# Optimization experiments

Hardware: AMD Instinct MI355X
Metric: run time of the kernel (lower is better)

Reference implementation:

```python
import jax, jax.numpy as jnp
import numpy as np
from jax import lax

SR = 4      # sr_ratio
HEADS = 8   # num_heads


def _upsample_bilinear_ac(x, out_h, out_w):
    # torch nn.Upsample(scale_factor=SR, mode='bilinear', align_corners=True)
    B, C, h, w = x.shape
    ys = jnp.linspace(0.0, h - 1.0, out_h)
    xs = jnp.linspace(0.0, w - 1.0, out_w)
    y0 = jnp.floor(ys).astype(jnp.int32)
    y1 = jnp.minimum(y0 + 1, h - 1)
    wy = (ys - y0).astype(x.dtype)
    x0 = jnp.floor(xs).astype(jnp.int32)
    x1 = jnp.minimum(x0 + 1, w - 1)
    wx = (xs - x0).astype(x.dtype)
    r = x[:, :, y0, :] * (1.0 - wy)[None, None, :, None] + x[:, :, y1, :] * wy[None, None, :, None]
    return r[:, :, :, x0] * (1.0 - wx) + r[:, :, :, x1] * wx


def _forward(x, sr_w, sr_b, ln_g, ln_b, q_w, k1_w, v1_w, k2_w, v2_w, proj_w, proj_b):
    B, C, H, W = x.shape
    ID = C // 4                      # internal_dim
    hd = ID // HEADS                 # head_dim
    scale = float(hd) ** -0.5
    # spatial-reduction conv for Q path: [B, ID, H/4, W/4]
    qf = lax.conv_general_dilated(x, sr_w, (SR, SR), 'VALID',
                                  dimension_numbers=('NCHW', 'OIHW', 'NCHW'))
    qf = qf + sr_b[None, :, None, None]
    Hs, Ws = qf.shape[2], qf.shape[3]
    N = Hs * Ws
    qf = qf.reshape(B, ID, N).transpose(0, 2, 1)          # [B, N, ID]
    # LayerNorm
    mu = qf.mean(-1, keepdims=True)
    var = qf.var(-1, keepdims=True)
    qn = (qf - mu) / jnp.sqrt(var + 1e-5) * ln_g + ln_b
    q = qn @ q_w                                          # [B, N, ID]
    # max / avg pooled K,V inputs: [B, N, C]
    xm = lax.reduce_window(x, -jnp.inf, lax.max, (1, 1, SR, SR), (1, 1, SR, SR), 'VALID')
    xm = xm.reshape(B, C, N).transpose(0, 2, 1)
    xa = lax.reduce_window(x, 0.0, lax.add, (1, 1, SR, SR), (1, 1, SR, SR), 'VALID') / float(SR * SR)
    xa = xa.reshape(B, C, N).transpose(0, 2, 1)

    def heads(t):
        return t.reshape(B, N, HEADS, hd).transpose(0, 2, 1, 3)  # [B, H, N, hd]

    qh = heads(q)
    k1, v1 = heads(xm @ k1_w), heads(xm @ v1_w)
    k2, v2 = heads(xa @ k2_w), heads(xa @ v2_w)

    def attend(k, v):
        a = jax.nn.softmax(jnp.einsum('bhnd,bhmd->bhnm', qh, k) * scale, axis=-1)
        return jnp.einsum('bhnm,bhmd->bhnd', a, v)

    z = attend(k1, v1) + attend(k2, v2)                   # [B, H, N, hd]
    z = z.transpose(0, 2, 1, 3).reshape(B, N, ID)
    z = z @ proj_w + proj_b                               # [B, N, C]
    z = z.transpose(0, 2, 1).reshape(B, C, Hs, Ws)
    return _upsample_bilinear_ac(z, H, W)


def setup_inputs() -> dict:
    key = jax.random.key(0)
    ks = jax.random.split(key, 9)
    B, C, H, W = 16, 256, 112, 112
    ID = C // 4

    def n(k, shape, s=0.02):
        return jax.random.normal(k, shape, jnp.float32) * s

    return {
        'x': jax.random.normal(ks[0], (B, C, H, W), jnp.float32),
        'sr_w': n(ks[1], (ID, C, SR, SR)),
        'sr_b': jnp.zeros((ID,), jnp.float32),
        'ln_g': jnp.ones((ID,), jnp.float32),
        'ln_b': jnp.zeros((ID,), jnp.float32),
        'q_w': n(ks[2], (ID, ID)),
        'k1_w': n(ks[3], (C, ID)),
        'v1_w': n(ks[4], (C, ID)),
        'k2_w': n(ks[5], (C, ID)),
        'v2_w': n(ks[6], (C, ID)),
        'proj_w': n(ks[7], (ID, C)),
        'proj_b': jnp.zeros((C,), jnp.float32),
    }


def reference(x, sr_w, sr_b, ln_g, ln_b, q_w, k1_w, v1_w, k2_w, v2_w, proj_w, proj_b):
    return _forward(x, sr_w, sr_b, ln_g, ln_b, q_w, k1_w, v1_w, k2_w, v2_w, proj_w, proj_b)
```

## Files before the change

### kernel.cpp

```cpp
#include <hip/hip_runtime.h>
#include <math.h>

typedef __attribute__((ext_vector_type(8))) short short8;
typedef __attribute__((ext_vector_type(4))) short bh4;
typedef __attribute__((ext_vector_type(4))) float f32x4;
typedef __attribute__((ext_vector_type(2))) unsigned uint2v;
typedef __attribute__((ext_vector_type(4))) unsigned uint4v;

#define MFMA16(A,B,C) __builtin_amdgcn_mfma_f32_16x16x32_bf16(A,B,C,0,0,0)

#if __has_builtin(__builtin_amdgcn_mfma_f32_16x16x16bf16_1k)
#define MFMA16x16(A,B,C) __builtin_amdgcn_mfma_f32_16x16x16bf16_1k(A,B,C,0,0,0)
#else
__device__ __forceinline__ f32x4 mfma16x16_asm(bh4 a, bh4 b, f32x4 c){
    asm volatile("v_mfma_f32_16x16x16_bf16 %0, %1, %2, %0" : "+v"(c) : "v"(a), "v"(b));
    return c;
}
#define MFMA16x16(A,B,C) mfma16x16_asm(A,B,C)
#endif

__device__ __forceinline__ unsigned short f2b(float f){
    unsigned u = __builtin_bit_cast(unsigned, f);
    return (unsigned short)((u + 0x7fffu + ((u>>16)&1u)) >> 16);
}
__device__ __forceinline__ unsigned pk2(float a, float b){
    return (unsigned)f2b(a) | ((unsigned)f2b(b) << 16);
}
__device__ __forceinline__ unsigned pk2rn(float a, float b){
    unsigned ua = __builtin_bit_cast(unsigned, a) + 0x8000u;
    unsigned ub = __builtin_bit_cast(unsigned, b) + 0x8000u;
    return (ua >> 16) | (ub & 0xffff0000u);
}


__global__ __launch_bounds__(256) void ktw(const float* __restrict__ srw,
    const float* __restrict__ qw, const float* __restrict__ k1w,
    const float* __restrict__ v1w, const float* __restrict__ k2w,
    const float* __restrict__ v2w, char* __restrict__ srwb,
    char* __restrict__ Wtm, char* __restrict__ Wta, char* __restrict__ QWt)
{
    int blk = blockIdx.x, t = threadIdx.x;
    if (blk < 128){
        int base = blk*2048 + t*8;
        float4 a = *(const float4*)(srw + base);
        float4 b = *(const float4*)(srw + base + 4);
        uint4 u = { pk2(a.x,a.y), pk2(a.z,a.w), pk2(b.x,b.y), pk2(b.z,b.w) };
        *(uint4*)(srwb + (size_t)base*2) = u;
    } else if (blk < 136){
        __shared__ float T[256*33];
        int idx = blk - 128, fi = idx >> 1, half = idx & 1;
        const float* src = (fi==0) ? k1w : (fi==1) ? v1w : (fi==2) ? k2w : v2w;
        char* dst = ((fi < 2) ? Wtm : Wta) + (size_t)((fi & 1)*64 + half*32) * 512;
        for (int li = t; li < 8192; li += 256){
            int c = li >> 5, o = li & 31;
            T[c*33 + o] = src[c*64 + half*32 + o];
        }
        __syncthreads();
        for (int lo = t; lo < 1024; lo += 256){
            int o = lo >> 5, c8 = lo & 31;
            float v[8];
            #pragma unroll
            for (int k = 0; k < 8; ++k) v[k] = T[(c8*8 + k)*33 + o];
            uint4 u = { pk2(v[0],v[1]), pk2(v[2],v[3]), pk2(v[4],v[5]), pk2(v[6],v[7]) };
            *(uint4*)(dst + o*512 + c8*16) = u;
        }
    } else {
        __shared__ float T[64*65];
        for (int li = t; li < 4096; li += 256)
            T[(li >> 6)*65 + (li & 63)] = qw[li];
        __syncthreads();
        for (int lo = t; lo < 512; lo += 256){
            int o = lo >> 3, i8 = lo & 7;
            float v[8];
            #pragma unroll
            for (int k = 0; k < 8; ++k) v[k] = T[(i8*8 + k)*65 + o];
            uint4 u = { pk2(v[0],v[1]), pk2(v[2],v[3]), pk2(v[4],v[5]), pk2(v[6],v[7]) };
            *(uint4*)(QWt + o*128 + i8*16) = u;
        }
    }
}

__global__ __launch_bounds__(256, 4) void k1(const float* __restrict__ x,
    const char* __restrict__ srwb, char* __restrict__ R, float* __restrict__ pws)
{
    __shared__ float pm[28*66];
    __shared__ float pa[28*66];
    int blk = blockIdx.x;
    int b = blk / 112, r5 = blk % 112, hs = r5 >> 2, cg4 = r5 & 3;
    int t = threadIdx.x;
    int w = t >> 6, l = t & 63, lr = l & 15, lg = l >> 4;
    int cpar = lg >> 1, r0 = (lg & 1) * 2;
    f32x4 acc0 = {0.f,0.f,0.f,0.f}, acc1 = {0.f,0.f,0.f,0.f};
    const float* xc = x + (size_t)(b*256 + cg4*64)*12544 + (size_t)(hs*4 + r0)*112;
    const char* Brow = srwb + (size_t)(w*16 + lr)*8192 + cg4*2048 + lg*16;
    int p0 = lr, p1 = min(16 + lr, 27);

    f32x4 A0,A1,A2,A3; uint4v Ba;
    f32x4 C0,C1,C2,C3; uint4v Bc;
    f32x4 D0,D1,D2,D3; uint4v Bd;
    f32x4 E0,E1,E2,E3; uint4v Be;

#define ISSUE(Xa,Xb,Xc,Xd,Bv,KS) do{ \
    const float* _s = xc + (size_t)((KS)*2 + cpar)*12544; \
    const char*  _bp = Brow + (KS)*64; \
    asm volatile("global_load_dwordx4 %0, %1, off" : "=&v"(Xa) : "v"(_s + p0*4)); \
    asm volatile("global_load_dwordx4 %0, %1, off" : "=&v"(Xb) : "v"(_s + 112 + p0*4)); \
    asm volatile("global_load_dwordx4 %0, %1, off" : "=&v"(Xc) : "v"(_s + p1*4)); \
    asm volatile("global_load_dwordx4 %0, %1, off" : "=&v"(Xd) : "v"(_s + 112 + p1*4)); \
    asm volatile("global_load_dwordx4 %0, %1, off" : "=&v"(Bv) : "v"(_bp)); }while(0)

#define WAITN(N) do{ asm volatile("s_waitcnt vmcnt(" #N ")" ::: "memory"); \
                     __builtin_amdgcn_sched_barrier(0); }while(0)

#define COMP(Xa,Xb,Xc,Xd,Bv,KS) do{ \
    if (w == 0){ \
        float mx0 = fmaxf(fmaxf(fmaxf(Xa[0],Xa[1]),fmaxf(Xa[2],Xa[3])), \
                          fmaxf(fmaxf(Xb[0],Xb[1]),fmaxf(Xb[2],Xb[3]))); \
        float sm0 = (Xa[0]+Xa[1])+(Xa[2]+Xa[3])+(Xb[0]+Xb[1])+(Xb[2]+Xb[3]); \
        float mx1 = fmaxf(fmaxf(fmaxf(Xc[0],Xc[1]),fmaxf(Xc[2],Xc[3])), \
                          fmaxf(fmaxf(Xd[0],Xd[1]),fmaxf(Xd[2],Xd[3]))); \
        float sm1 = (Xc[0]+Xc[1])+(Xc[2]+Xc[3])+(Xd[0]+Xd[1])+(Xd[2]+Xd[3]); \
        mx0 = fmaxf(mx0, __shfl_xor(mx0, 16, 64)); \
        sm0 = sm0 + __shfl_xor(sm0, 16, 64); \
        mx1 = fmaxf(mx1, __shfl_xor(mx1, 16, 64)); \
        sm1 = sm1 + __shfl_xor(sm1, 16, 64); \
        if ((lg & 1) == 0){ \
            int c = (KS)*2 + cpar; \
            pm[p0*66 + c] = mx0; pa[p0*66 + c] = sm0 * (1.f/16.f); \
            if (lr < 12){ pm[p1*66 + c] = mx1; pa[p1*66 + c] = sm1 * (1.f/16.f); } \
        } \
    } \
    short8 af0 = __builtin_bit_cast(short8, \
        (uint4v){ pk2(Xa[0],Xa[1]), pk2(Xa[2],Xa[3]), pk2(Xb[0],Xb[1]), pk2(Xb[2],Xb[3]) }); \
    short8 af1 = __builtin_bit_cast(short8, \
        (uint4v){ pk2(Xc[0],Xc[1]), pk2(Xc[2],Xc[3]), pk2(Xd[0],Xd[1]), pk2(Xd[2],Xd[3]) }); \
    short8 bf = __builtin_bit_cast(short8, Bv); \
    acc0 = MFMA16(af0, bf, acc0); \
    acc1 = MFMA16(af1, bf, acc1); }while(0)

    ISSUE(A0,A1,A2,A3,Ba, 0);
    ISSUE(C0,C1,C2,C3,Bc, 1);
    ISSUE(D0,D1,D2,D3,Bd, 2);
    ISSUE(E0,E1,E2,E3,Be, 3);
    #pragma unroll 1
    for (int it = 0; it < 7; ++it){
        int s4 = it*4;
        WAITN(15); COMP(A0,A1,A2,A3,Ba, s4+0); ISSUE(A0,A1,A2,A3,Ba, s4+4);
        WAITN(15); COMP(C0,C1,C2,C3,Bc, s4+1); ISSUE(C0,C1,C2,C3,Bc, s4+5);
        WAITN(15); COMP(D0,D1,D2,D3,Bd, s4+2); ISSUE(D0,D1,D2,D3,Bd, s4+6);
        WAITN(15); COMP(E0,E1,E2,E3,Be, s4+3); ISSUE(E0,E1,E2,E3,Be, s4+7);
    }
    WAITN(15); COMP(A0,A1,A2,A3,Ba, 28);
    WAITN(10); COMP(C0,C1,C2,C3,Bc, 29);
    WAITN(5);  COMP(D0,D1,D2,D3,Bd, 30);
    WAITN(0);  COMP(E0,E1,E2,E3,Be, 31);

#undef ISSUE
#undef WAITN
#undef COMP

    size_t rowB = (size_t)b*784 + hs*28;
    float* pp = pws + (size_t)((b*28 + hs)*4 + cg4)*1792;
    #pragma unroll
    for (int rg = 0; rg < 4; ++rg){
        int m0 = lg*4 + rg, m1 = 16 + lg*4 + rg;
        pp[m0*64 + w*16 + lr] = acc0[rg];
        if (m1 < 28) pp[m1*64 + w*16 + lr] = acc1[rg];
    }
    __syncthreads();
    if (t < 224){
        int m = t >> 3, sub = t & 7;
        float vm[8], va8[8];
        #pragma unroll
        for (int k = 0; k < 8; ++k){
            vm[k]  = pm[m*66 + sub*8 + k];
            va8[k] = pa[m*66 + sub*8 + k];
        }
        uint4 um = { pk2(vm[0],vm[1]), pk2(vm[2],vm[3]), pk2(vm[4],vm[5]), pk2(vm[6],vm[7]) };
        uint4 ua = { pk2(va8[0],va8[1]), pk2(va8[2],va8[3]), pk2(va8[4],va8[5]), pk2(va8[6],va8[7]) };
        *(uint4*)(R + (rowB + m)*1024 + cg4*128 + sub*16)       = um;
        *(uint4*)(R + (rowB + m)*1024 + 512 + cg4*128 + sub*16) = ua;
    }
}

__global__ __launch_bounds__(512) void k2(const float* __restrict__ pws_,
    const float* __restrict__ srb, const float* __restrict__ lng,
    const float* __restrict__ lnb, const char* __restrict__ Wtm,
    const char* __restrict__ Wta, const char* __restrict__ QWt,
    char* __restrict__ R)
{
    __shared__ __align__(16) char PM[16384];
    __shared__ __align__(16) char PA[16384];
    __shared__ float Db[32*64];
    __shared__ __align__(16) char QN[4096];
    int blk = blockIdx.x, b = blk/28, hs = blk%28;
    int t = threadIdx.x, w = t>>6, l = t&63, lr = l&15, lg = l>>4;
    size_t rowB = (size_t)b*784 + hs*28;
    const char* Rb = R + rowB*1024;
    for (int li = t; li < 896; li += 512){
        int m = li >> 5, c16 = li & 31;
        uint4 vm = *(const uint4*)(Rb + (size_t)m*1024 + c16*16);
        uint4 va = *(const uint4*)(Rb + (size_t)m*1024 + 512 + c16*16);
        int dst = m*512 + ((c16*16) ^ ((m&7)<<4));
        *(uint4*)(PM + dst) = vm;
        *(uint4*)(PA + dst) = va;
    }
    const float* p0 = pws_ + (size_t)(b*28 + hs)*4*1792;
    for (int e = t; e < 1792; e += 512)
        Db[e] = ((p0[e] + p0[1792+e]) + (p0[3584+e] + p0[5376+e])) + srb[e & 63];
    __syncthreads();
    float g = lng[l], be = lnb[l];
    #pragma unroll
    for (int i = 0; i < 4; ++i){
        int m = w + i*8;
        float v = Db[m*64 + l];
        float s = v, ss = v*v;
        #pragma unroll
        for (int off = 1; off < 64; off <<= 1){
            s  += __shfl_xor(s,  off, 64);
            ss += __shfl_xor(ss, off, 64);
        }
        float mu = s * (1.f/64.f);
        float var = ss * (1.f/64.f) - mu*mu;
        float qn = (v - mu) * rsqrtf(var + 1e-5f) * g + be;
        *(unsigned short*)(QN + m*128 + ((l*2) ^ ((m&7)<<4))) = f2b(qn);
    }
    __syncthreads();
    int fam = w >> 2, ofp = w & 3;
    const char* PMA = fam ? PA : PM;
    const char* Wt  = fam ? Wta : Wtm;
    f32x4 a00={0.f,0.f,0.f,0.f}, a01=a00, a10=a00, a11=a00;
    int swzr = (lr & 7) << 4;
    #pragma unroll
    for (int ks = 0; ks < 8; ++ks){
        int kb = ks*64 + lg*16;
        short8 x0 = *(const short8*)(PMA + lr*512 + (kb ^ swzr));
        short8 x1 = *(const short8*)(PMA + (16+lr)*512 + (kb ^ swzr));
        short8 b0 = *(const short8*)(Wt + (size_t)(ofp*32 + lr)*512 + kb);
        short8 b1 = *(const short8*)(Wt + (size_t)(ofp*32 + 16 + lr)*512 + kb);
        a00 = MFMA16(x0, b0, a00); a01 = MFMA16(x0, b1, a01);
        a10 = MFMA16(x1, b0, a10); a11 = MFMA16(x1, b1, a11);
    }
    f32x4 q0={0.f,0.f,0.f,0.f}, q1=q0;
    if (w < 4){
        #pragma unroll
        for (int ks = 0; ks < 2; ++ks){
            int kb = ks*64 + lg*16;
            short8 xa_ = *(const short8*)(QN + lr*128 + (kb ^ swzr));
            short8 xb_ = *(const short8*)(QN + (16+lr)*128 + (kb ^ swzr));
            short8 bq  = *(const short8*)(QWt + (size_t)(w*16 + lr)*128 + kb);
            q0 = MFMA16(xa_, bq, q0);
            q1 = MFMA16(xb_, bq, q1);
        }
    }
    #pragma unroll
    for (int j = 0; j < 2; ++j){
        int o128 = ofp*32 + j*16 + lr;
        int o = o128 & 63, hh = o >> 3, dd = o & 7, mat = fam*2 + (o128 >> 6);
        int byteoff = 128 + hh*64 + mat*16 + dd*2;
        f32x4 am  = j ? a01 : a00;
        f32x4 am1 = j ? a11 : a10;
        #pragma unroll
        for (int rg = 0; rg < 4; ++rg){
            int m0 = lg*4 + rg, m1 = 16 + lg*4 + rg;
            *(unsigned short*)(R + (rowB + m0)*1024 + byteoff) = f2b(am[rg]);
            if (m1 < 28)
                *(unsigned short*)(R + (rowB + m1)*1024 + byteoff) = f2b(am1[rg]);
        }
    }
    if (w < 4){
        int o = w*16 + lr;
        #pragma unroll
        for (int rg = 0; rg < 4; ++rg){
            int m0 = lg*4 + rg, m1 = 16 + lg*4 + rg;
            *(unsigned short*)(R + (rowB + m0)*1024 + o*2) = f2b(q0[rg]);
            if (m1 < 28)
                *(unsigned short*)(R + (rowB + m1)*1024 + o*2) = f2b(q1[rg]);
        }
    }
}

__global__ __launch_bounds__(256) void kattn(const char* __restrict__ R, float* __restrict__ z)
{
    __shared__ __align__(16) char QT [6144];
    __shared__ __align__(16) char K1b[5376];
    __shared__ __align__(16) char K2b[5376];
    __shared__ __align__(16) char VT1[3840];
    __shared__ __align__(16) char VT2[3840];
    int blk = blockIdx.x;
    int bh = blk / 7, nseg = blk % 7;
    int b = bh >> 3, h = bh & 7;
    int t = threadIdx.x, w = t >> 6, l = t & 63;
    int col = l & 15, g = l >> 4;

    for (int i = t; i < 384; i += 256) ((uint4*)QT)[i] = uint4{0,0,0,0};
    for (int i = t; i < 112; i += 256){
        *(uint4*)(K1b + i*48 + 16) = uint4{0,0,0,0};
        *(uint4*)(K2b + i*48 + 16) = uint4{0,0,0,0};
    }
    for (int i = t; i < 120; i += 256){
        *(uint4*)(VT1 + 1920 + i*16) = uint4{0,0,0,0};
        *(uint4*)(VT2 + 1920 + i*16) = uint4{0,0,0,0};
    }
    __syncthreads();
    if (t < 112){
        uint4 qv = *(const uint4*)(R + ((size_t)b*784 + nseg*112 + t)*1024 + h*16);
        *(uint2*)(QT + t*48)     = uint2{qv.x, qv.y};
        *(uint2*)(QT + t*48 + 8) = uint2{qv.z, qv.w};
    }
    __syncthreads();

    bh4 qf[2];
    #pragma unroll
    for (int nf = 0; nf < 2; ++nf)
        qf[nf] = *(const bh4*)(QT + (w*28 + nf*16 + col)*48 + g*8);

    f32x4 o1[2] = {{0,0,0,0},{0,0,0,0}}, o2[2] = {{0,0,0,0},{0,0,0,0}};
    float d1[2] = {0.f,0.f}, d2[2] = {0.f,0.f};
    const float C2 = 0.51004244f;

    for (int mt = 0; mt < 7; ++mt){
        __syncthreads();
        for (int li = t; li < 448; li += 256){
            int m = li >> 2, part = li & 3;
            uint4 v = *(const uint4*)(R + ((size_t)b*784 + mt*112 + m)*1024 + 128 + h*64 + part*16);
            if ((part & 1) == 0){
                char* Kb = (part == 0) ? K1b : K2b;
                *(uint2*)(Kb + m*48)     = uint2{v.x, v.y};
                *(uint2*)(Kb + m*48 + 8) = uint2{v.z, v.w};
            } else {
                char* Vb = (part == 1) ? VT1 : VT2;
                unsigned arr[4] = {v.x, v.y, v.z, v.w};
                #pragma unroll
                for (int d = 0; d < 4; ++d){
                    *(unsigned short*)(Vb + (d*2)*240   + m*2) = (unsigned short)(arr[d] & 0xffffu);
                    *(unsigned short*)(Vb + (d*2+1)*240 + m*2) = (unsigned short)(arr[d] >> 16);
                }
            }
        }
        __syncthreads();
        #pragma unroll
        for (int mc = 0; mc < 7; ++mc){
            bh4 ka = *(const bh4*)(K1b + (mc*16 + col)*48 + g*8);
            bh4 kb = *(const bh4*)(K2b + (mc*16 + col)*48 + g*8);
            bh4 va = *(const bh4*)(VT1 + col*240 + mc*32 + g*8);
            bh4 vb = *(const bh4*)(VT2 + col*240 + mc*32 + g*8);
            #pragma unroll
            for (int nf = 0; nf < 2; ++nf){
                f32x4 zr = {0.f,0.f,0.f,0.f};
                f32x4 s1 = MFMA16x16(ka, qf[nf], zr);
                float p0 = exp2f(s1[0]*C2), p1 = exp2f(s1[1]*C2);
                float p2 = exp2f(s1[2]*C2), p3 = exp2f(s1[3]*C2);
                d1[nf] += (p0+p1)+(p2+p3);
                bh4 pf1 = __builtin_bit_cast(bh4, (uint2v){pk2rn(p0,p1), pk2rn(p2,p3)});
                o1[nf] = MFMA16x16(va, pf1, o1[nf]);
                f32x4 s2 = MFMA16x16(kb, qf[nf], zr);
                float r0 = exp2f(s2[0]*C2), r1 = exp2f(s2[1]*C2);
                float r2 = exp2f(s2[2]*C2), r3 = exp2f(s2[3]*C2);
                d2[nf] += (r0+r1)+(r2+r3);
                bh4 pf2 = __builtin_bit_cast(bh4, (uint2v){pk2rn(r0,r1), pk2rn(r2,r3)});
                o2[nf] = MFMA16x16(vb, pf2, o2[nf]);
            }
        }
    }
    #pragma unroll
    for (int nf = 0; nf < 2; ++nf){
        d1[nf] += __shfl_xor(d1[nf], 16, 64); d1[nf] += __shfl_xor(d1[nf], 32, 64);
        d2[nf] += __shfl_xor(d2[nf], 16, 64); d2[nf] += __shfl_xor(d2[nf], 32, 64);
    }
    if (g < 2){
        #pragma unroll
        for (int nf = 0; nf < 2; ++nf){
            if (nf == 1 && col >= 12) continue;
            int n = nseg*112 + w*28 + nf*16 + col;
            float ra = 1.f / d1[nf], rb = 1.f / d2[nf];
            float4 ov;
            ov.x = o1[nf][0]*ra + o2[nf][0]*rb;
            ov.y = o1[nf][1]*ra + o2[nf][1]*rb;
            ov.z = o1[nf][2]*ra + o2[nf][2]*rb;
            ov.w = o1[nf][3]*ra + o2[nf][3]*rb;
            *(float4*)(z + ((size_t)b*784 + n)*64 + h*8 + g*4) = ov;
        }
    }
}

__global__ __launch_bounds__(256) void kpu(const float* __restrict__ z,
    const float* __restrict__ pw, const float* __restrict__ pb,
    float* __restrict__ out)
{
    __shared__ float plane[8*784];
    __shared__ float wsl[64*8];
    __shared__ int   ti0[112];
    __shared__ float twv[112];
    int blk = blockIdx.x;
    int b = blk >> 5, cg = blk & 31;
    int t = threadIdx.x;
    if (t < 128){
        #pragma unroll
        for (int q = 0; q < 4; ++q){
            int idx = t*4 + q; int o = idx >> 3, j = idx & 7;
            wsl[o*8 + j] = pw[o*256 + cg*8 + j];
        }
    }
    if (t < 112){
        float s = (float)t * (27.f/111.f);
        int i0 = (int)s; if (i0 > 27) i0 = 27;
        ti0[t] = i0; twv[t] = s - (float)i0;
    }
    __syncthreads();
    {
        int nh = t >> 1, jh = (t & 1) * 4;
        float bias0 = pb[cg*8 + jh], bias1 = pb[cg*8 + jh + 1];
        float bias2 = pb[cg*8 + jh + 2], bias3 = pb[cg*8 + jh + 3];
        for (int n = nh; n < 784; n += 128){
            const float* zr = z + ((size_t)b*784 + n)*64;
            float a0 = bias0, a1 = bias1, a2 = bias2, a3 = bias3;
            #pragma unroll
            for (int o4 = 0; o4 < 16; ++o4){
                float4 zv = *(const float4*)(zr + o4*4);
                const float* wr = wsl + (o4*4)*8 + jh;
                a0 = fmaf(zv.x, wr[0],  a0); a1 = fmaf(zv.x, wr[1],  a1);
                a2 = fmaf(zv.x, wr[2],  a2); a3 = fmaf(zv.x, wr[3],  a3);
                a0 = fmaf(zv.y, wr[8],  a0); a1 = fmaf(zv.y, wr[9],  a1);
                a2 = fmaf(zv.y, wr[10], a2); a3 = fmaf(zv.y, wr[11], a3);
                a0 = fmaf(zv.z, wr[16], a0); a1 = fmaf(zv.z, wr[17], a1);
                a2 = fmaf(zv.z, wr[18], a2); a3 = fmaf(zv.z, wr[19], a3);
                a0 = fmaf(zv.w, wr[24], a0); a1 = fmaf(zv.w, wr[25], a1);
                a2 = fmaf(zv.w, wr[26], a2); a3 = fmaf(zv.w, wr[27], a3);
            }
            plane[(jh+0)*784 + n] = a0;
            plane[(jh+1)*784 + n] = a1;
            plane[(jh+2)*784 + n] = a2;
            plane[(jh+3)*784 + n] = a3;
        }
    }
    __syncthreads();
    float* ob = out + ((size_t)b*256 + cg*8)*12544;
    for (int i = t; i < 12544; i += 256){
        int y = i/112, xx = i%112;
        int y0 = ti0[y], x0 = ti0[xx];
        float wy = twv[y], wx = twv[xx];
        int y1 = min(y0+1, 27), x1 = min(x0+1, 27);
        int i00 = y0*28 + x0, i01 = y0*28 + x1, i10 = y1*28 + x0, i11 = y1*28 + x1;
        #pragma unroll
        for (int j = 0; j < 8; ++j){
            const float* pl = plane + j*784;
            float a  = pl[i00] + (pl[i10]-pl[i00])*wy;
            float bb = pl[i01] + (pl[i11]-pl[i01])*wy;
            ob[(size_t)j*12544 + i] = a + (bb-a)*wx;
        }
    }
}

extern "C" void kernel_launch(void* const* d_in, const int* in_sizes, int n_in,
                              void* d_out, int out_size, void* d_ws, size_t ws_size,
                              hipStream_t stream) {
    const float* x   = (const float*)d_in[0];
    const float* srw = (const float*)d_in[1];
    const float* srb = (const float*)d_in[2];
    const float* lng = (const float*)d_in[3];
    const float* lnb = (const float*)d_in[4];
    const float* qw  = (const float*)d_in[5];
    const float* k1w = (const float*)d_in[6];
    const float* v1w = (const float*)d_in[7];
    const float* k2w = (const float*)d_in[8];
    const float* v2w = (const float*)d_in[9];
    const float* pw  = (const float*)d_in[10];
    const float* pb  = (const float*)d_in[11];

    char*  Rws  = (char*)d_ws;
    float* pws  = (float*)(Rws + 12845056);
    char*  srwb = Rws + 25690112;
    char*  Wtm  = Rws + 26214400;
    char*  Wta  = Rws + 26279936;
    char*  QWt  = Rws + 26345472;
    float* z    = (float*)(Rws + 12845056);
    float* out  = (float*)d_out;

    ktw  <<<137,  256, 0, stream>>>(srw, qw, k1w, v1w, k2w, v2w, srwb, Wtm, Wta, QWt);
    k1   <<<1792, 256, 0, stream>>>(x, srwb, Rws, pws);
    k2   <<<448,  512, 0, stream>>>(pws, srb, lng, lnb, Wtm, Wta, QWt, Rws);
    kattn<<<896,  256, 0, stream>>>(Rws, z);
    kpu  <<<512,  256, 0, stream>>>(z, pw, pb, out);
}
```

Baseline: 270.6 us.

## Shrink k1 pipeline depth and LDS for occupancy, vectorize upsample stores

k1 now keeps two load stages in flight instead of four, which frees registers, and raises launch bounds from 4 to 6 blocks per SM. It also packs the max and avg pool values as bf16 pairs into one shared array, halving that LDS footprint. Separately, the final upsample loop handles four adjacent x positions per thread and writes them as float4 stores. The shallower prefetch leaves fewer loads outstanding per wave, so memory latency may be hidden worse unless the extra occupancy makes up for it.

New measurement: 268.7 us. About the same (-0.7%).

```diff
diff --git a/kernel.cpp b/kernel.cpp
--- a/kernel.cpp
+++ b/kernel.cpp
@@ -80,11 +80,10 @@
     }
 }
 
-__global__ __launch_bounds__(256, 4) void k1(const float* __restrict__ x,
+__global__ __launch_bounds__(256, 6) void k1(const float* __restrict__ x,
     const char* __restrict__ srwb, char* __restrict__ R, float* __restrict__ pws)
 {
-    __shared__ float pm[28*66];
-    __shared__ float pa[28*66];
+    __shared__ unsigned pmpa[28*66];
     int blk = blockIdx.x;
     int b = blk / 112, r5 = blk % 112, hs = r5 >> 2, cg4 = r5 & 3;
     int t = threadIdx.x;
@@ -97,8 +96,6 @@
 
     f32x4 A0,A1,A2,A3; uint4v Ba;
     f32x4 C0,C1,C2,C3; uint4v Bc;
-    f32x4 D0,D1,D2,D3; uint4v Bd;
-    f32x4 E0,E1,E2,E3; uint4v Be;
 
 #define ISSUE(Xa,Xb,Xc,Xd,Bv,KS) do{ \
     const float* _s = xc + (size_t)((KS)*2 + cpar)*12544; \
@@ -126,8 +123,8 @@
         sm1 = sm1 + __shfl_xor(sm1, 16, 64); \
         if ((lg & 1) == 0){ \
             int c = (KS)*2 + cpar; \
-            pm[p0*66 + c] = mx0; pa[p0*66 + c] = sm0 * (1.f/16.f); \
-            if (lr < 12){ pm[p1*66 + c] = mx1; pa[p1*66 + c] = sm1 * (1.f/16.f); } \
+            pmpa[p0*66 + c] = pk2(mx0, sm0 * (1.f/16.f)); \
+            if (lr < 12) pmpa[p1*66 + c] = pk2(mx1, sm1 * (1.f/16.f)); \
         } \
     } \
     short8 af0 = __builtin_bit_cast(short8, \
@@ -140,20 +137,14 @@
 
     ISSUE(A0,A1,A2,A3,Ba, 0);
     ISSUE(C0,C1,C2,C3,Bc, 1);
-    ISSUE(D0,D1,D2,D3,Bd, 2);
-    ISSUE(E0,E1,E2,E3,Be, 3);
     #pragma unroll 1
-    for (int it = 0; it < 7; ++it){
-        int s4 = it*4;
-        WAITN(15); COMP(A0,A1,A2,A3,Ba, s4+0); ISSUE(A0,A1,A2,A3,Ba, s4+4);
-        WAITN(15); COMP(C0,C1,C2,C3,Bc, s4+1); ISSUE(C0,C1,C2,C3,Bc, s4+5);
-        WAITN(15); COMP(D0,D1,D2,D3,Bd, s4+2); ISSUE(D0,D1,D2,D3,Bd, s4+6);
-        WAITN(15); COMP(E0,E1,E2,E3,Be, s4+3); ISSUE(E0,E1,E2,E3,Be, s4+7);
-    }
-    WAITN(15); COMP(A0,A1,A2,A3,Ba, 28);
-    WAITN(10); COMP(C0,C1,C2,C3,Bc, 29);
-    WAITN(5);  COMP(D0,D1,D2,D3,Bd, 30);
-    WAITN(0);  COMP(E0,E1,E2,E3,Be, 31);
+    for (int it = 0; it < 15; ++it){
+        int s2 = it*2;
+        WAITN(5); COMP(A0,A1,A2,A3,Ba, s2);   ISSUE(A0,A1,A2,A3,Ba, s2+2);
+        WAITN(5); COMP(C0,C1,C2,C3,Bc, s2+1); ISSUE(C0,C1,C2,C3,Bc, s2+3);
+    }
+    WAITN(5); COMP(A0,A1,A2,A3,Ba, 30);
+    WAITN(0); COMP(C0,C1,C2,C3,Bc, 31);
 
 #undef ISSUE
 #undef WAITN
@@ -170,14 +161,13 @@
     __syncthreads();
     if (t < 224){
         int m = t >> 3, sub = t & 7;
-        float vm[8], va8[8];
-        #pragma unroll
-        for (int k = 0; k < 8; ++k){
-            vm[k]  = pm[m*66 + sub*8 + k];
-            va8[k] = pa[m*66 + sub*8 + k];
-        }
-        uint4 um = { pk2(vm[0],vm[1]), pk2(vm[2],vm[3]), pk2(vm[4],vm[5]), pk2(vm[6],vm[7]) };
-        uint4 ua = { pk2(va8[0],va8[1]), pk2(va8[2],va8[3]), pk2(va8[4],va8[5]), pk2(va8[6],va8[7]) };
+        unsigned u[8];
+        #pragma unroll
+        for (int k = 0; k < 8; ++k) u[k] = pmpa[m*66 + sub*8 + k];
+        uint4 um = { (u[0]&0xffffu)|(u[1]<<16), (u[2]&0xffffu)|(u[3]<<16),
+                     (u[4]&0xffffu)|(u[5]<<16), (u[6]&0xffffu)|(u[7]<<16) };
+        uint4 ua = { (u[0]>>16)|(u[1]&0xffff0000u), (u[2]>>16)|(u[3]&0xffff0000u),
+                     (u[4]>>16)|(u[5]&0xffff0000u), (u[6]>>16)|(u[7]&0xffff0000u) };
         *(uint4*)(R + (rowB + m)*1024 + cg4*128 + sub*16)       = um;
         *(uint4*)(R + (rowB + m)*1024 + 512 + cg4*128 + sub*16) = ua;
     }
@@ -436,18 +426,31 @@
     }
     __syncthreads();
     float* ob = out + ((size_t)b*256 + cg*8)*12544;
-    for (int i = t; i < 12544; i += 256){
-        int y = i/112, xx = i%112;
-        int y0 = ti0[y], x0 = ti0[xx];
-        float wy = twv[y], wx = twv[xx];
-        int y1 = min(y0+1, 27), x1 = min(x0+1, 27);
-        int i00 = y0*28 + x0, i01 = y0*28 + x1, i10 = y1*28 + x0, i11 = y1*28 + x1;
+    for (int i4 = t; i4 < 3136; i4 += 256){
+        int y = i4 / 28, xq = (i4 % 28) * 4;
+        int y0 = ti0[y], y1 = min(y0+1, 27);
+        float wy = twv[y];
+        int x0q[4], x1q[4]; float wxq[4];
+        #pragma unroll
+        for (int qi = 0; qi < 4; ++qi){
+            int xx = xq + qi;
+            x0q[qi] = ti0[xx]; x1q[qi] = min(x0q[qi]+1, 27); wxq[qi] = twv[xx];
+        }
+        int base = y*112 + xq;
         #pragma unroll
         for (int j = 0; j < 8; ++j){
-            const float* pl = plane + j*784;
-            float a  = pl[i00] + (pl[i10]-pl[i00])*wy;
-            float bb = pl[i01] + (pl[i11]-pl[i01])*wy;
-            ob[(size_t)j*12544 + i] = a + (bb-a)*wx;
+            const float* r0p = plane + j*784 + y0*28;
+            const float* r1p = plane + j*784 + y1*28;
+            float4 ov;
+            #pragma unroll
+            for (int qi = 0; qi < 4; ++qi){
+                float a  = r0p[x0q[qi]] + (r1p[x0q[qi]] - r0p[x0q[qi]])*wy;
+                float bb = r0p[x1q[qi]] + (r1p[x1q[qi]] - r0p[x1q[qi]])*wy;
+                float v = a + (bb - a)*wxq[qi];
+                if (qi == 0) ov.x = v; else if (qi == 1) ov.y = v;
+                else if (qi == 2) ov.z = v; else ov.w = v;
+            }
+            *(float4*)(ob + (size_t)j*12544 + base) = ov;
         }
     }
 }
```
